# Optimization experiments

Hardware: AMD Instinct MI355X
Metric: run time of the kernel (lower is better)

The kernel has to match this reference:

```python
import jax, jax.numpy as jnp
import numpy as np

B, C, N, CIN, COUT, ORDER = 16, 32, 207, 64, 64, 2
SCALE = COUT / (ORDER * CIN)          # = 0.5
BN_EVAL = 1.0 / np.sqrt(1.0 + 1e-5)   # eval-mode BatchNorm2d at init (mean=0, var=1)


def setup_inputs() -> dict:
    key = jax.random.key(0)
    ks = jax.random.split(key, 9)
    s = 0.05  # xavier-ish small init scale
    return {
        "x":          jax.random.normal(ks[0], (B, C, N, CIN), dtype=jnp.float32),
        "res_weight": jax.random.normal(ks[1], (C, N, CIN, COUT, ORDER), dtype=jnp.float32) * s,
        "res_bias":   jax.random.normal(ks[2], (1, C, N, 1, 1), dtype=jnp.float32) * s,
        "mlp_w":      jax.random.normal(ks[3], (COUT, CIN), dtype=jnp.float32) * s,
        "mlp_b":      jax.random.normal(ks[4], (COUT,), dtype=jnp.float32) * s,
        "gate_w":     jax.random.normal(ks[5], (COUT, CIN), dtype=jnp.float32) * s,
        "gate_b":     jax.random.normal(ks[6], (COUT,), dtype=jnp.float32) * s,
        "order_w":    jax.random.normal(ks[7], (ORDER,), dtype=jnp.float32) * s,
        "order_b":    jax.random.normal(ks[8], (1,), dtype=jnp.float32) * s,
    }


def reference(x, res_weight, res_bias, mlp_w, mlp_b, gate_w, gate_b, order_w, order_b):
    # shared linear branch (dropout = identity in eval)
    x_share = jnp.einsum('bcni,oi->bcno', x, mlp_w) + mlp_b            # [B,C,N,COUT]
    # polynomial features: h[..., 0]=x, h[..., 1]=BN(x*x) (eval BN ~ identity scale)
    x1 = (x * x) * BN_EVAL
    h = jnp.stack([x, x1], axis=-1)                                    # [B,C,N,CIN,ORDER]
    # per-(channel,node) grouped linear
    x_uniq = jnp.einsum('bcnid,cniod->bcnod', h, res_weight) + res_bias  # [B,C,N,COUT,ORDER]
    # order_mlp: Linear(order -> 1), squeeze
    x_uniq = jnp.einsum('bcnod,d->bcno', x_uniq, order_w) + order_b    # [B,C,N,COUT]
    x_uniq = x_uniq * (SCALE / 4.0)
    # sigmoid gate combine + residual
    gate = jax.nn.sigmoid(jnp.einsum('bcni,oi->bcno', x, gate_w) + gate_b)
    return gate * x_uniq + (1.0 - gate) * x_share + x
```

## Files before the change

kernel.cpp:

```cpp
#include <hip/hip_runtime.h>

#define Bdim 16
#define Cdim 32
#define Ndim 207
#define X_B (Cdim * Ndim * 64)
#define X_C (Ndim * 64)
#define W_C (Ndim * 64 * 64 * 2)
#define W_N (64 * 64 * 2)
#define BN_EVAL 0.9999950000374997f

using s8v = __attribute__((ext_vector_type(8))) short;
using f4v = __attribute__((ext_vector_type(4))) float;

union UV { uint4 u; s8v s; };

__device__ __forceinline__ unsigned pk(float lo, float hi) {
    union { float f; unsigned u; } a, b;
    a.f = lo; b.f = hi;
    return __builtin_amdgcn_perm(b.u, a.u, 0x07060302u);
}

__global__ __launch_bounds__(256, 4)
void fused_ml_mfma(const float* __restrict__ x,
                   const float* __restrict__ rw,
                   const float* __restrict__ rb,
                   const float* __restrict__ mw,
                   const float* __restrict__ mb,
                   const float* __restrict__ gw,
                   const float* __restrict__ gb,
                   const float* __restrict__ ow,
                   const float* __restrict__ obp,
                   float* __restrict__ out)
{
    __shared__ unsigned short A1[16 * 136];
    __shared__ unsigned short A2[16 * 72];
    __shared__ unsigned short MG[128 * 72];

    const int cn = blockIdx.x, c = cn / Ndim, n = cn % Ndim;
    const int t = threadIdx.x;
    const float ow0 = ow[0], ow1 = ow[1];
    const float bnow1 = ow1 * BN_EVAL;

    {
        const int b = t >> 4, i0 = (t & 15) * 4;
        const float* xrow = x + (size_t)b * X_B + (size_t)c * X_C + n * 64;
        const float4 xv = *(const float4*)(xrow + i0);
        uint4 v;
        v.x = pk(xv.x * ow0, xv.x * xv.x * bnow1);
        v.y = pk(xv.y * ow0, xv.y * xv.y * bnow1);
        v.z = pk(xv.z * ow0, xv.z * xv.z * bnow1);
        v.w = pk(xv.w * ow0, xv.w * xv.w * bnow1);
        *(uint4*)&A1[b * 136 + i0 * 2] = v;
        uint2 p;
        p.x = pk(xv.x, xv.y);
        p.y = pk(xv.z, xv.w);
        *(uint2*)&A2[b * 72 + i0] = p;
    }
    {
        const int r = t >> 1, h = t & 1;
        const float* src = (r < 64 ? mw + r * 64 : gw + (r - 64) * 64) + h * 32;
        unsigned short* dst = &MG[r * 72 + h * 32];
#pragma unroll
        for (int u = 0; u < 4; ++u) {
            const float4 a4 = ((const float4*)src)[2 * u];
            const float4 b4 = ((const float4*)src)[2 * u + 1];
            uint4 v;
            v.x = pk(a4.x, a4.y); v.y = pk(a4.z, a4.w);
            v.z = pk(b4.x, b4.y); v.w = pk(b4.z, b4.w);
            *(uint4*)&dst[u * 8] = v;
        }
    }
    __syncthreads();

    const int l = t & 63, w = t >> 6, q = l >> 4, nn = l & 15;
    const int o = w * 16 + nn;
    const float* wtile = rw + (size_t)c * W_C + (size_t)n * W_N + o * 2;

    f4v accU = {0.f, 0.f, 0.f, 0.f};
    f4v accM = {0.f, 0.f, 0.f, 0.f};
    f4v accG = {0.f, 0.f, 0.f, 0.f};

#pragma unroll
    for (int s = 0; s < 4; ++s) {
        const float* gp = wtile + (size_t)(16 * s + 4 * q) * 128;
        const float2 w0 = *(const float2*)(gp);
        const float2 w1 = *(const float2*)(gp + 128);
        const float2 w2 = *(const float2*)(gp + 256);
        const float2 w3 = *(const float2*)(gp + 384);
        UV bu;
        bu.u.x = pk(w0.x, w0.y); bu.u.y = pk(w1.x, w1.y);
        bu.u.z = pk(w2.x, w2.y); bu.u.w = pk(w3.x, w3.y);
        UV au; au.u = *(const uint4*)&A1[nn * 136 + 32 * s + 8 * q];
        accU = __builtin_amdgcn_mfma_f32_16x16x32_bf16(au.s, bu.s, accU, 0, 0, 0);
    }
#pragma unroll
    for (int s = 0; s < 2; ++s) {
        UV a2u; a2u.u = *(const uint4*)&A2[nn * 72 + 32 * s + 8 * q];
        UV bm;  bm.u  = *(const uint4*)&MG[o * 72 + 32 * s + 8 * q];
        UV bg2; bg2.u = *(const uint4*)&MG[(64 + o) * 72 + 32 * s + 8 * q];
        accM = __builtin_amdgcn_mfma_f32_16x16x32_bf16(a2u.s, bm.s,  accM, 0, 0, 0);
        accG = __builtin_amdgcn_mfma_f32_16x16x32_bf16(a2u.s, bg2.s, accG, 0, 0, 0);
    }

    const float rbias = rb[c * Ndim + n];
    const float uconst = rbias * (ow0 + ow1) + obp[0];
    const float mbias = mb[o], gbias = gb[o];
    const float* xcol = x + (size_t)c * X_C + n * 64 + o;
    float* ocol = out + (size_t)c * X_C + n * 64 + o;
#pragma unroll
    for (int r = 0; r < 4; ++r) {
        const int b = q * 4 + r;
        const float uniq = (accU[r] + uconst) * 0.125f;
        const float xs = accM[r] + mbias;
        const float g = 1.f / (1.f + __expf(-(accG[r] + gbias)));
        const float xres = xcol[(size_t)b * X_B];
        ocol[(size_t)b * X_B] = g * uniq + (1.f - g) * xs + xres;
    }
}

extern "C" void kernel_launch(void* const* d_in, const int* in_sizes, int n_in,
                              void* d_out, int out_size, void* d_ws, size_t ws_size,
                              hipStream_t stream)
{
    const float* x   = (const float*)d_in[0];
    const float* rw  = (const float*)d_in[1];
    const float* rb  = (const float*)d_in[2];
    const float* mw  = (const float*)d_in[3];
    const float* mb  = (const float*)d_in[4];
    const float* gw  = (const float*)d_in[5];
    const float* gb  = (const float*)d_in[6];
    const float* ow  = (const float*)d_in[7];
    const float* ob  = (const float*)d_in[8];
    float* out = (float*)d_out;

    fused_ml_mfma<<<dim3(Cdim * Ndim), dim3(256), 0, stream>>>(
        x, rw, rb, mw, mb, gw, gb, ow, ob, out);
}
```

Measured before the change: 334.9 us.

## Drop LDS staging and load MFMA operands directly from global memory

Removes the shared-memory staging of x features and the mlp/gate weight matrices, along with the block-wide barrier. Each lane now loads its MFMA A and B fragments straight from global memory and converts them to bf16 in registers. The launch-bounds occupancy hint is also raised from 4 to 6 blocks per CU. The cost is redundant global loads of x and the small weight matrices across the four waves, which are expected to be served from cache, plus possible register pressure under the tighter bound.

```diff
diff --git a/kernel.cpp b/kernel.cpp
--- a/kernel.cpp
+++ b/kernel.cpp
@@ -20,7 +20,7 @@
     return __builtin_amdgcn_perm(b.u, a.u, 0x07060302u);
 }
 
-__global__ __launch_bounds__(256, 4)
+__global__ __launch_bounds__(256, 6)
 void fused_ml_mfma(const float* __restrict__ x,
                    const float* __restrict__ rw,
                    const float* __restrict__ rb,
@@ -32,48 +32,15 @@
                    const float* __restrict__ obp,
                    float* __restrict__ out)
 {
-    __shared__ unsigned short A1[16 * 136];
-    __shared__ unsigned short A2[16 * 72];
-    __shared__ unsigned short MG[128 * 72];
-
     const int cn = blockIdx.x, c = cn / Ndim, n = cn % Ndim;
     const int t = threadIdx.x;
+    const int l = t & 63, w = t >> 6, q = l >> 4, nn = l & 15;
+    const int o = w * 16 + nn;
+
     const float ow0 = ow[0], ow1 = ow[1];
     const float bnow1 = ow1 * BN_EVAL;
 
-    {
-        const int b = t >> 4, i0 = (t & 15) * 4;
-        const float* xrow = x + (size_t)b * X_B + (size_t)c * X_C + n * 64;
-        const float4 xv = *(const float4*)(xrow + i0);
-        uint4 v;
-        v.x = pk(xv.x * ow0, xv.x * xv.x * bnow1);
-        v.y = pk(xv.y * ow0, xv.y * xv.y * bnow1);
-        v.z = pk(xv.z * ow0, xv.z * xv.z * bnow1);
-        v.w = pk(xv.w * ow0, xv.w * xv.w * bnow1);
-        *(uint4*)&A1[b * 136 + i0 * 2] = v;
-        uint2 p;
-        p.x = pk(xv.x, xv.y);
-        p.y = pk(xv.z, xv.w);
-        *(uint2*)&A2[b * 72 + i0] = p;
-    }
-    {
-        const int r = t >> 1, h = t & 1;
-        const float* src = (r < 64 ? mw + r * 64 : gw + (r - 64) * 64) + h * 32;
-        unsigned short* dst = &MG[r * 72 + h * 32];
-#pragma unroll
-        for (int u = 0; u < 4; ++u) {
-            const float4 a4 = ((const float4*)src)[2 * u];
-            const float4 b4 = ((const float4*)src)[2 * u + 1];
-            uint4 v;
-            v.x = pk(a4.x, a4.y); v.y = pk(a4.z, a4.w);
-            v.z = pk(b4.x, b4.y); v.w = pk(b4.z, b4.w);
-            *(uint4*)&dst[u * 8] = v;
-        }
-    }
-    __syncthreads();
-
-    const int l = t & 63, w = t >> 6, q = l >> 4, nn = l & 15;
-    const int o = w * 16 + nn;
+    const float* xrow  = x + (size_t)nn * X_B + (size_t)c * X_C + n * 64;
     const float* wtile = rw + (size_t)c * W_C + (size_t)n * W_N + o * 2;
 
     f4v accU = {0.f, 0.f, 0.f, 0.f};
@@ -82,7 +49,15 @@
 
 #pragma unroll
     for (int s = 0; s < 4; ++s) {
-        const float* gp = wtile + (size_t)(16 * s + 4 * q) * 128;
+        const int i0 = 16 * s + 4 * q;
+        const float4 xv = *(const float4*)(xrow + i0);
+        UV au;
+        au.u.x = pk(xv.x * ow0, xv.x * xv.x * bnow1);
+        au.u.y = pk(xv.y * ow0, xv.y * xv.y * bnow1);
+        au.u.z = pk(xv.z * ow0, xv.z * xv.z * bnow1);
+        au.u.w = pk(xv.w * ow0, xv.w * xv.w * bnow1);
+
+        const float* gp = wtile + (size_t)i0 * 128;
         const float2 w0 = *(const float2*)(gp);
         const float2 w1 = *(const float2*)(gp + 128);
         const float2 w2 = *(const float2*)(gp + 256);
@@ -90,16 +65,33 @@
         UV bu;
         bu.u.x = pk(w0.x, w0.y); bu.u.y = pk(w1.x, w1.y);
         bu.u.z = pk(w2.x, w2.y); bu.u.w = pk(w3.x, w3.y);
-        UV au; au.u = *(const uint4*)&A1[nn * 136 + 32 * s + 8 * q];
+
         accU = __builtin_amdgcn_mfma_f32_16x16x32_bf16(au.s, bu.s, accU, 0, 0, 0);
     }
+
 #pragma unroll
     for (int s = 0; s < 2; ++s) {
-        UV a2u; a2u.u = *(const uint4*)&A2[nn * 72 + 32 * s + 8 * q];
-        UV bm;  bm.u  = *(const uint4*)&MG[o * 72 + 32 * s + 8 * q];
-        UV bg2; bg2.u = *(const uint4*)&MG[(64 + o) * 72 + 32 * s + 8 * q];
-        accM = __builtin_amdgcn_mfma_f32_16x16x32_bf16(a2u.s, bm.s,  accM, 0, 0, 0);
-        accG = __builtin_amdgcn_mfma_f32_16x16x32_bf16(a2u.s, bg2.s, accG, 0, 0, 0);
+        const int i0 = 32 * s + 8 * q;
+        const float4 xa = *(const float4*)(xrow + i0);
+        const float4 xb = *(const float4*)(xrow + i0 + 4);
+        UV a2;
+        a2.u.x = pk(xa.x, xa.y); a2.u.y = pk(xa.z, xa.w);
+        a2.u.z = pk(xb.x, xb.y); a2.u.w = pk(xb.z, xb.w);
+
+        const float4 m0 = *(const float4*)(mw + o * 64 + i0);
+        const float4 m1 = *(const float4*)(mw + o * 64 + i0 + 4);
+        UV bm;
+        bm.u.x = pk(m0.x, m0.y); bm.u.y = pk(m0.z, m0.w);
+        bm.u.z = pk(m1.x, m1.y); bm.u.w = pk(m1.z, m1.w);
+
+        const float4 g0 = *(const float4*)(gw + o * 64 + i0);
+        const float4 g1 = *(const float4*)(gw + o * 64 + i0 + 4);
+        UV bg2;
+        bg2.u.x = pk(g0.x, g0.y); bg2.u.y = pk(g0.z, g0.w);
+        bg2.u.z = pk(g1.x, g1.y); bg2.u.w = pk(g1.z, g1.w);
+
+        accM = __builtin_amdgcn_mfma_f32_16x16x32_bf16(a2.s, bm.s,  accM, 0, 0, 0);
+        accG = __builtin_amdgcn_mfma_f32_16x16x32_bf16(a2.s, bg2.s, accG, 0, 0, 0);
     }
 
     const float rbias = rb[c * Ndim + n];
```

Measured after the change: 348.4 us. +4.0%, slower.
